# Optimization experiments

Hardware: AMD Instinct MI355X
Metric: run time of the kernel (lower is better)

## Reference

```python
import jax, jax.numpy as jnp
import numpy as np

B, LQ, LKV = 32, 512, 512
SIZE, H = 512, 8
HD = SIZE // H
SCALE = 1.0 / np.sqrt(HD)
LN_EPS = 1e-5


def layer_norm(x, w, b):
    mu = jnp.mean(x, axis=-1, keepdims=True)
    var = jnp.mean(jnp.square(x - mu), axis=-1, keepdims=True)
    return (x - mu) * jax.lax.rsqrt(var + LN_EPS) * w + b


def setup_inputs() -> dict:
    key = jax.random.key(0)
    ks = jax.random.split(key, 8)
    s = 0.02
    return {
        "query": jax.random.normal(ks[0], (B, LQ, SIZE), jnp.float32),
        "key_value": jax.random.normal(ks[1], (B, LKV, SIZE), jnp.float32),
        "Wq": jax.random.normal(ks[2], (SIZE, SIZE), jnp.float32) * s,
        "bq": jnp.zeros((SIZE,), jnp.float32),
        "Wk": jax.random.normal(ks[3], (SIZE, SIZE), jnp.float32) * s,
        "bk": jnp.zeros((SIZE,), jnp.float32),
        "Wv": jax.random.normal(ks[4], (SIZE, SIZE), jnp.float32) * s,
        "bv": jnp.zeros((SIZE,), jnp.float32),
        "Wo": jax.random.normal(ks[5], (SIZE, SIZE), jnp.float32) * s,
        "bo": jnp.zeros((SIZE,), jnp.float32),
        "ln0_w": jnp.ones((SIZE,), jnp.float32),
        "ln0_b": jnp.zeros((SIZE,), jnp.float32),
        "ln1_w": jnp.ones((SIZE,), jnp.float32),
        "ln1_b": jnp.zeros((SIZE,), jnp.float32),
    }


def reference(query, key_value, Wq, bq, Wk, bk, Wv, bv, Wo, bo, ln0_w, ln0_b, ln1_w, ln1_b):
    b, lq, _ = query.shape
    lkv = key_value.shape[1]
    # projections
    q = query @ Wq.T + bq          # [B, Lq, SIZE]
    k = key_value @ Wk.T + bk      # [B, Lkv, SIZE]
    v = key_value @ Wv.T + bv
    # split heads: torch cat(split(head_size, 2), 0) == [B,L,H,HD] view with head axis separate
    qh = q.reshape(b, lq, H, HD)
    kh = k.reshape(b, lkv, H, HD)
    vh = v.reshape(b, lkv, H, HD)
    # attention scores [B, H, Lq, Lkv]
    A_ = jnp.einsum("bqhd,bkhd->bhqk", qh, kh) * SCALE
    # signed softmax: tanh(A_) * softmax(sqrt(A_^2 + 0.01)) over keys
    A = jnp.tanh(A_) * jax.nn.softmax(jnp.sqrt(jnp.square(A_) + 0.01), axis=-1)
    # residual q + attention output, merge heads back
    oh = qh + jnp.einsum("bhqk,bkhd->bqhd", A, vh)   # [B, Lq, H, HD]
    output = oh.reshape(b, lq, SIZE)
    output = layer_norm(output, ln0_w, ln0_b)
    output = output + jax.nn.relu(output @ Wo.T + bo)
    output = layer_norm(output, ln1_w, ln1_b)
    return output
```

## Files before the change

### kernel.cpp

```cpp
#include <hip/hip_runtime.h>

#define SIZE_D 512
#define HEADS  8
#define HDIM   64
#define BATCH  32
#define SEQ    512
#define SCALE_F 0.125f
#define NROWS  (BATCH * SEQ)

typedef __attribute__((ext_vector_type(8))) short bf16x8;
typedef __attribute__((ext_vector_type(4))) float f32x4;
typedef __attribute__((ext_vector_type(4))) unsigned int u32x4;

__device__ __forceinline__ unsigned short f2bf(float f) {
    union { float f; unsigned int u; } c{f};
    unsigned int x = c.u;
    x += 0x7fffu + ((x >> 16) & 1u);
    return (unsigned short)(x >> 16);
}
__device__ __forceinline__ float bf2f(unsigned short u) {
    union { unsigned int i; float f; } c;
    c.i = (unsigned int)u << 16;
    return c.f;
}
__device__ __forceinline__ unsigned int pack2bf(float lo, float hi) {
    return ((__float_as_uint(hi) + 0x8000u) & 0xffff0000u) |
           ((__float_as_uint(lo) + 0x8000u) >> 16);
}
__device__ __forceinline__ void gload_lds16(const unsigned short* g, unsigned short* l) {
    __builtin_amdgcn_global_load_lds(
        (const __attribute__((address_space(1))) unsigned int*)g,
        (__attribute__((address_space(3))) unsigned int*)l, 16, 0, 0);
}

__global__ __launch_bounds__(256) void cvt_w4(const float* __restrict__ w0,
                                              const float* __restrict__ w1,
                                              const float* __restrict__ w2,
                                              const float* __restrict__ w3,
                                              unsigned short* __restrict__ d) {
    const float* srcs[4] = {w0, w1, w2, w3};
    const float* s = srcs[blockIdx.y];
    unsigned short* dst = d + (size_t)blockIdx.y * (SIZE_D * SIZE_D);
    const int n = SIZE_D * SIZE_D;
    const int stride = gridDim.x * blockDim.x * 4;
    for (int i = (blockIdx.x * blockDim.x + threadIdx.x) * 4; i < n; i += stride) {
        const float4 v = *reinterpret_cast<const float4*>(s + i);
        ushort4 o;
        o.x = f2bf(v.x); o.y = f2bf(v.y); o.z = f2bf(v.z); o.w = f2bf(v.w);
        *reinterpret_cast<ushort4*>(dst + i) = o;
    }
}

__global__ __launch_bounds__(256, 2) void gemm_proj3(const float* __restrict__ query,
                                                     const float* __restrict__ keyv,
                                                     const unsigned short* __restrict__ Wall,
                                                     const float* __restrict__ bq,
                                                     const float* __restrict__ bk,
                                                     const float* __restrict__ bv,
                                                     unsigned short* __restrict__ Qh,
                                                     unsigned short* __restrict__ Kh,
                                                     unsigned short* __restrict__ Vt) {
    __shared__ __align__(16) unsigned short Ad[4][128 * 32];
    __shared__ __align__(16) unsigned short Bd[4][128 * 32];

    const int tid  = threadIdx.x;
    const int wv   = tid >> 6;
    const int lane = tid & 63;
    const int g    = lane >> 4;
    const int y    = blockIdx.y;
    const int bm   = blockIdx.x * 128;
    const int bn   = y * 128;
    const int wr   = wv >> 1;
    const int wc   = wv & 1;

    const float* A = (y < 4) ? query : keyv;

    float4 areg[2][2][2];

    auto loadA = [&](int t, int slot) {
        const int k0 = t * 32;
#pragma unroll
        for (int i = 0; i < 2; ++i) {
            const int o   = i * 4096 + tid * 16;
            const int row = o >> 6;
            const int col = ((o & 63) ^ (((row >> 1) & 3) << 4)) >> 1;
            const float* src = A + (size_t)(bm + row) * SIZE_D + k0 + col;
            areg[slot][i][0] = *reinterpret_cast<const float4*>(src);
            areg[slot][i][1] = *reinterpret_cast<const float4*>(src + 4);
        }
    };
    auto writeA = [&](int buf, int slot) {
#pragma unroll
        for (int i = 0; i < 2; ++i) {
            const int o = i * 4096 + tid * 16;
            union { unsigned int u[4]; bf16x8 v; } pk;
            pk.u[0] = pack2bf(areg[slot][i][0].x, areg[slot][i][0].y);
            pk.u[1] = pack2bf(areg[slot][i][0].z, areg[slot][i][0].w);
            pk.u[2] = pack2bf(areg[slot][i][1].x, areg[slot][i][1].y);
            pk.u[3] = pack2bf(areg[slot][i][1].z, areg[slot][i][1].w);
            *reinterpret_cast<bf16x8*>(&Ad[buf][o >> 1]) = pk.v;
        }
    };
    auto stageW = [&](int buf, int t) {
        const int k0 = t * 32;
#pragma unroll
        for (int i = 0; i < 2; ++i) {
            const int o   = i * 4096 + tid * 16;
            const int row = o >> 6;
            const int col = ((o & 63) ^ (((row >> 1) & 3) << 4)) >> 1;
            gload_lds16(Wall + (size_t)(bn + row) * SIZE_D + k0 + col, &Bd[buf][o >> 1]);
        }
    };

    f32x4 acc[4][4];
#pragma unroll
    for (int mt = 0; mt < 4; ++mt)
#pragma unroll
        for (int nt = 0; nt < 4; ++nt) acc[mt][nt] = (f32x4){0.f, 0.f, 0.f, 0.f};

    auto compute = [&](int buf) {
        bf16x8 af[4], bfr[4];
#pragma unroll
        for (int mt = 0; mt < 4; ++mt) {
            const int r = wr * 64 + mt * 16 + (lane & 15);
            int byte = r * 64 + g * 16;
            byte ^= ((r >> 1) & 3) << 4;
            af[mt] = *reinterpret_cast<const bf16x8*>(
                reinterpret_cast<const char*>(&Ad[buf][0]) + byte);
        }
#pragma unroll
        for (int nt = 0; nt < 4; ++nt) {
            const int r = wc * 64 + nt * 16 + (lane & 15);
            int byte = r * 64 + g * 16;
            byte ^= ((r >> 1) & 3) << 4;
            bfr[nt] = *reinterpret_cast<const bf16x8*>(
                reinterpret_cast<const char*>(&Bd[buf][0]) + byte);
        }
#pragma unroll
        for (int mt = 0; mt < 4; ++mt)
#pragma unroll
            for (int nt = 0; nt < 4; ++nt)
                acc[mt][nt] = __builtin_amdgcn_mfma_f32_16x16x32_bf16(
                    af[mt], bfr[nt], acc[mt][nt], 0, 0, 0);
    };

    loadA(0, 0);
    loadA(1, 1);
    stageW(0, 0);
    stageW(1, 1);
    writeA(0, 0);
    writeA(1, 1);
    __syncthreads();

    for (int tt = 0; tt < 16; tt += 2) {
        if (tt < 14) {
            loadA(tt + 2, 0);
            loadA(tt + 3, 1);
            stageW((tt + 2) & 3, tt + 2);
            stageW((tt + 3) & 3, tt + 3);
        }

        compute(tt & 3);
        if (tt < 14) writeA((tt + 2) & 3, 0);
        compute((tt + 1) & 3);
        if (tt < 14) writeA((tt + 3) & 3, 1);

        __syncthreads();
    }

    if (y < 8) {
        const float* bias = (y < 4) ? bq : bk;
        unsigned short* D = (y < 4) ? Qh : Kh;
        const int coff = (y < 4) ? 0 : 512;
#pragma unroll
        for (int nt = 0; nt < 4; ++nt) {
            const int colL = bn - coff + wc * 64 + nt * 16 + (lane & 15);
            const float bc = bias[colL];
            const int h = colL >> 6, dd = colL & 63;
#pragma unroll
            for (int mt = 0; mt < 4; ++mt) {
                const int row0 = bm + wr * 64 + mt * 16 + g * 4;
#pragma unroll
                for (int r = 0; r < 4; ++r) {
                    const int row = row0 + r;
                    const int b_ = row >> 9, l = row & 511;
                    float z = acc[mt][nt][r] + bc;
                    if (y >= 4) z *= SCALE_F;
                    D[(((size_t)b_ * HEADS + h) * SEQ + l) * HDIM + dd] = f2bf(z);
                }
            }
        }
    } else {
#pragma unroll
        for (int nt = 0; nt < 4; ++nt) {
            const int c2 = bn - 1024 + wc * 64 + nt * 16 + (lane & 15);
            const float bc = bv[c2];
            const int hV = c2 >> 6, dV = c2 & 63;
#pragma unroll
            for (int mt = 0; mt < 4; ++mt) {
                const int row0 = bm + wr * 64 + mt * 16 + g * 4;
                const int b_ = row0 >> 9, kv = row0 & 511;
                ushort4 pk;
                pk.x = f2bf(acc[mt][nt][0] + bc);
                pk.y = f2bf(acc[mt][nt][1] + bc);
                pk.z = f2bf(acc[mt][nt][2] + bc);
                pk.w = f2bf(acc[mt][nt][3] + bc);
                *reinterpret_cast<ushort4*>(
                    &Vt[(((size_t)b_ * HEADS + hV) * HDIM + dV) * SEQ + kv]) = pk;
            }
        }
    }
}

__global__ __launch_bounds__(256, 2) void attn_mfma(const unsigned short* __restrict__ Qh,
                                                    const unsigned short* __restrict__ Kh,
                                                    const unsigned short* __restrict__ Vt,
                                                    unsigned short* __restrict__ outb) {
    __shared__ __align__(16) unsigned short Kt[4][64 * 64];
    __shared__ __align__(16) unsigned short Vs[4][64 * 64];

    const int tid  = threadIdx.x;
    const int wv   = tid >> 6;
    const int lane = tid & 63;
    const int bh   = blockIdx.x;
    const int b    = bh >> 3;
    const int h    = bh & 7;
    const int g    = lane >> 4;

    const unsigned short* Qb = Qh + (size_t)bh * (SEQ * HDIM);
    const unsigned short* Kb = Kh + (size_t)bh * (SEQ * HDIM);
    const unsigned short* Vb = Vt + (size_t)bh * (HDIM * SEQ);

    const int m0 = blockIdx.y * 256 + wv * 64;

    auto stageKV = [&](int buf, int t) {
        const int kv0 = t * 64;
#pragma unroll
        for (int i = 0; i < 2; ++i) {
            const int o   = i * 4096 + tid * 16;
            const int row = o >> 7;
            const int in  = (o & 127) ^ ((row & 7) << 4);
            gload_lds16(Kb + (size_t)(kv0 + row) * HDIM + (in >> 1), &Kt[buf][o >> 1]);
            gload_lds16(Vb + (size_t)row * SEQ + kv0 + (in >> 1), &Vs[buf][o >> 1]);
        }
    };

    bf16x8 qf[4][2];
#pragma unroll
    for (int mt = 0; mt < 4; ++mt)
#pragma unroll
        for (int kc = 0; kc < 2; ++kc) {
            const int m = m0 + mt * 16 + (lane & 15);
            union { u32x4 u; bf16x8 v; } cv;
            cv.u = *reinterpret_cast<const u32x4*>(
                Qb + (size_t)m * HDIM + kc * 32 + g * 8);
            qf[mt][kc] = cv.v;
        }

    f32x4 oacc[4][4];
    float esum[4] = {0.f, 0.f, 0.f, 0.f};
#pragma unroll
    for (int mt = 0; mt < 4; ++mt)
#pragma unroll
        for (int x = 0; x < 4; ++x) oacc[mt][x] = (f32x4){0.f, 0.f, 0.f, 0.f};

    stageKV(0, 0);
    stageKV(1, 1);
    __syncthreads();

    for (int tt = 0; tt < 8; tt += 2) {
        if (tt < 6) {
            stageKV((tt + 2) & 3, tt + 2);
            stageKV((tt + 3) & 3, tt + 3);
        }

#pragma unroll
        for (int p = 0; p < 2; ++p) {
            const int cur = (tt + p) & 3;

            f32x4 sacc[4][4];
#pragma unroll
            for (int nt = 0; nt < 4; ++nt)
#pragma unroll
                for (int mt = 0; mt < 4; ++mt) sacc[nt][mt] = (f32x4){0.f, 0.f, 0.f, 0.f};

#pragma unroll
            for (int kc = 0; kc < 2; ++kc) {
                bf16x8 kf[4];
#pragma unroll
                for (int nt = 0; nt < 4; ++nt) {
                    const int kvl = nt * 16 + (lane & 15);
                    int byte = kvl * 128 + kc * 64 + g * 16;
                    byte ^= (kvl & 7) << 4;
                    kf[nt] = *reinterpret_cast<const bf16x8*>(
                        reinterpret_cast<const char*>(&Kt[cur][0]) + byte);
                }
                __builtin_amdgcn_s_setprio(1);
#pragma unroll
                for (int nt = 0; nt < 4; ++nt)
#pragma unroll
                    for (int mt = 0; mt < 4; ++mt)
                        sacc[nt][mt] = __builtin_amdgcn_mfma_f32_16x16x32_bf16(
                            kf[nt], qf[mt][kc], sacc[nt][mt], 0, 0, 0);
                __builtin_amdgcn_s_setprio(0);
            }

            bf16x8 pa[2][4];
#pragma unroll
            for (int c = 0; c < 2; ++c)
#pragma unroll
                for (int mt = 0; mt < 4; ++mt) {
                    float w[8];
#pragma unroll
                    for (int j = 0; j < 8; ++j) {
                        const float s  = sacc[2 * c + (j >> 2)][mt][j & 3];
                        const float a  = fabsf(s);
                        const float tt_ = __expf(a);
                        const float t2 = tt_ * tt_;
                        const float u  = __builtin_amdgcn_sqrtf(fmaf(s, s, 0.01f));
                        const float dl = u - a;
                        const float ed = fmaf(dl, fmaf(dl, 0.5f, 1.0f), 1.0f);
                        const float eu = tt_ * ed;
                        esum[mt] += eu;
                        const float th = fmaf(-2.0f, __builtin_amdgcn_rcpf(t2 + 1.0f), 1.0f);
                        w[j] = __builtin_copysignf(th * eu, s);
                    }
                    union { unsigned int u[4]; bf16x8 v; } pk;
#pragma unroll
                    for (int pp = 0; pp < 4; ++pp)
                        pk.u[pp] = (__float_as_uint(w[2 * pp + 1]) & 0xffff0000u) |
                                   (__float_as_uint(w[2 * pp]) >> 16);
                    pa[c][mt] = pk.v;
                }

#pragma unroll
            for (int c = 0; c < 2; ++c) {
                bf16x8 vf[4];
#pragma unroll
                for (int dt = 0; dt < 4; ++dt) {
                    const int d = dt * 16 + (lane & 15);
                    const int swz = (d & 7) << 4;
                    const int rowb = d * 128;
                    uint2 lo = *reinterpret_cast<const uint2*>(
                        reinterpret_cast<const char*>(&Vs[cur][0]) +
                        (rowb + (((c * 32 + 4 * g) * 2) ^ swz)));
                    uint2 hi = *reinterpret_cast<const uint2*>(
                        reinterpret_cast<const char*>(&Vs[cur][0]) +
                        (rowb + (((c * 32 + 16 + 4 * g) * 2) ^ swz)));
                    union { unsigned int u[4]; bf16x8 v; } cvb;
                    cvb.u[0] = lo.x; cvb.u[1] = lo.y;
                    cvb.u[2] = hi.x; cvb.u[3] = hi.y;
                    vf[dt] = cvb.v;
                }
                __builtin_amdgcn_s_setprio(1);
#pragma unroll
                for (int mt = 0; mt < 4; ++mt)
#pragma unroll
                    for (int dt = 0; dt < 4; ++dt)
                        oacc[mt][dt] = __builtin_amdgcn_mfma_f32_16x16x32_bf16(
                            pa[c][mt], vf[dt], oacc[mt][dt], 0, 0, 0);
                __builtin_amdgcn_s_setprio(0);
            }
        }

        __syncthreads();
    }

    float rden[4];
#pragma unroll
    for (int mt = 0; mt < 4; ++mt) {
        float e = esum[mt];
        e += __shfl_xor(e, 16);
        e += __shfl_xor(e, 32);
        rden[mt] = __builtin_amdgcn_rcpf(e);
    }
    float rr_[4][4];
#pragma unroll
    for (int mt = 0; mt < 4; ++mt)
#pragma unroll
        for (int r = 0; r < 4; ++r)
            rr_[mt][r] = __shfl(rden[mt], g * 4 + r);

#pragma unroll
    for (int mt = 0; mt < 4; ++mt)
#pragma unroll
        for (int dt = 0; dt < 4; ++dt)
#pragma unroll
            for (int r = 0; r < 4; ++r) {
                const int m = m0 + mt * 16 + g * 4 + r;
                const int d = dt * 16 + (lane & 15);
                const float qv = bf2f(Qb[(size_t)m * HDIM + d]);
                outb[((size_t)b * SEQ + m) * SIZE_D + h * HDIM + d] =
                    f2bf(qv + oacc[mt][dt][r] * rr_[mt][r]);
            }
}

__global__ __launch_bounds__(256) void ln0_bf16(const unsigned short* __restrict__ in,
                                                const float* __restrict__ w,
                                                const float* __restrict__ b,
                                                unsigned short* __restrict__ outb) {
    const int tid  = threadIdx.x;
    const int lane = tid & 63;
    const int row  = blockIdx.x * 4 + (tid >> 6);
    const size_t base = (size_t)row * SIZE_D + lane * 8;

    const ushort4 a0 = *reinterpret_cast<const ushort4*>(&in[base]);
    const ushort4 a1 = *reinterpret_cast<const ushort4*>(&in[base + 4]);
    float x[8];
    x[0] = bf2f(a0.x); x[1] = bf2f(a0.y); x[2] = bf2f(a0.z); x[3] = bf2f(a0.w);
    x[4] = bf2f(a1.x); x[5] = bf2f(a1.y); x[6] = bf2f(a1.z); x[7] = bf2f(a1.w);

    float s = 0.f, sq = 0.f;
#pragma unroll
    for (int j = 0; j < 8; ++j) { s += x[j]; sq += x[j] * x[j]; }
#pragma unroll
    for (int off = 32; off > 0; off >>= 1) {
        s  += __shfl_xor(s, off);
        sq += __shfl_xor(sq, off);
    }

    const float mu  = s * (1.0f / SIZE_D);
    const float var = sq * (1.0f / SIZE_D) - mu * mu;
    const float rr  = rsqrtf(var + 1e-5f);

    const float4 w0 = *reinterpret_cast<const float4*>(&w[lane * 8]);
    const float4 w1 = *reinterpret_cast<const float4*>(&w[lane * 8 + 4]);
    const float4 b0 = *reinterpret_cast<const float4*>(&b[lane * 8]);
    const float4 b1 = *reinterpret_cast<const float4*>(&b[lane * 8 + 4]);
    const float wa[8] = {w0.x, w0.y, w0.z, w0.w, w1.x, w1.y, w1.z, w1.w};
    const float ba[8] = {b0.x, b0.y, b0.z, b0.w, b1.x, b1.y, b1.z, b1.w};

    union { unsigned short s[8]; bf16x8 v; } o;
#pragma unroll
    for (int j = 0; j < 8; ++j)
        o.s[j] = f2bf((x[j] - mu) * rr * wa[j] + ba[j]);
    *reinterpret_cast<bf16x8*>(&outb[base]) = o.v;
}

__global__ __launch_bounds__(512, 2) void oproj_ln(const unsigned short* __restrict__ X,
                                                   const unsigned short* __restrict__ W,
                                                   const float* __restrict__ bo,
                                                   const float* __restrict__ g1,
                                                   const float* __restrict__ b1,
                                                   float* __restrict__ out) {
    __shared__ __align__(16) unsigned short Ad[2][32 * 32];
    __shared__ __align__(16) unsigned short Bd[2][512 * 32];
    __shared__ float red[32][8][2];
    __shared__ float stat[32][2];

    const int tid  = threadIdx.x;
    const int wv   = tid >> 6;
    const int lane = tid & 63;
    const int bm   = blockIdx.x * 32;

    auto stage = [&](int buf, int t) {
        const int k0 = t * 32;
        if (tid < 128) {
            const int o   = tid * 16;
            const int row = o >> 6;
            const int in  = (o & 63) ^ (((row >> 1) & 3) << 4);
            gload_lds16(X + (size_t)(bm + row) * SIZE_D + k0 + (in >> 1), &Ad[buf][o >> 1]);
        }
#pragma unroll
        for (int i = 0; i < 4; ++i) {
            const int o   = i * 8192 + tid * 16;
            const int row = o >> 6;
            const int in  = (o & 63) ^ (((row >> 1) & 3) << 4);
            gload_lds16(W + (size_t)row * SIZE_D + k0 + (in >> 1), &Bd[buf][o >> 1]);
        }
    };

    f32x4 acc[2][4];
#pragma unroll
    for (int mt = 0; mt < 2; ++mt)
#pragma unroll
        for (int nt = 0; nt < 4; ++nt) acc[mt][nt] = (f32x4){0.f, 0.f, 0.f, 0.f};

    stage(0, 0);
    __syncthreads();
    int cur = 0;

    for (int t = 0; t < 16; ++t) {
        if (t < 15) stage(cur ^ 1, t + 1);

        bf16x8 af[2], bfr[4];
#pragma unroll
        for (int mt = 0; mt < 2; ++mt) {
            const int r = mt * 16 + (lane & 15);
            int byte = r * 64 + (lane >> 4) * 16;
            byte ^= ((r >> 1) & 3) << 4;
            af[mt] = *reinterpret_cast<const bf16x8*>(
                reinterpret_cast<const char*>(&Ad[cur][0]) + byte);
        }
#pragma unroll
        for (int nt = 0; nt < 4; ++nt) {
            const int r = wv * 64 + nt * 16 + (lane & 15);
            int byte = r * 64 + (lane >> 4) * 16;
            byte ^= ((r >> 1) & 3) << 4;
            bfr[nt] = *reinterpret_cast<const bf16x8*>(
                reinterpret_cast<const char*>(&Bd[cur][0]) + byte);
        }
#pragma unroll
        for (int mt = 0; mt < 2; ++mt)
#pragma unroll
            for (int nt = 0; nt < 4; ++nt)
                acc[mt][nt] = __builtin_amdgcn_mfma_f32_16x16x32_bf16(
                    af[mt], bfr[nt], acc[mt][nt], 0, 0, 0);

        __syncthreads();
        cur ^= 1;
    }

#pragma unroll
    for (int nt = 0; nt < 4; ++nt) {
        const int n  = wv * 64 + nt * 16 + (lane & 15);
        const float bc = bo[n];
#pragma unroll
        for (int mt = 0; mt < 2; ++mt) {
            const int row0 = bm + mt * 16 + (lane >> 4) * 4;
#pragma unroll
            for (int r = 0; r < 4; ++r) {
                const float R = bf2f(X[(size_t)(row0 + r) * SIZE_D + n]);
                acc[mt][nt][r] = R + fmaxf(acc[mt][nt][r] + bc, 0.0f);
            }
        }
    }

    float ps[2][4], pq[2][4];
#pragma unroll
    for (int mt = 0; mt < 2; ++mt)
#pragma unroll
        for (int r = 0; r < 4; ++r) {
            float s = 0.f, q = 0.f;
#pragma unroll
            for (int nt = 0; nt < 4; ++nt) {
                const float v = acc[mt][nt][r];
                s += v; q += v * v;
            }
#pragma unroll
            for (int off = 1; off <= 8; off <<= 1) {
                s += __shfl_xor(s, off);
                q += __shfl_xor(q, off);
            }
            ps[mt][r] = s; pq[mt][r] = q;
        }
    if ((lane & 15) < 8) {
        const int mtw = (lane & 15) >> 2;
        const int rw  = lane & 3;
        const int rowL = mtw * 16 + (lane >> 4) * 4 + rw;
        red[rowL][wv][0] = ps[mtw][rw];
        red[rowL][wv][1] = pq[mtw][rw];
    }
    __syncthreads();
    if (tid < 32) {
        float s = 0.f, q = 0.f;
#pragma unroll
        for (int w8 = 0; w8 < 8; ++w8) { s += red[tid][w8][0]; q += red[tid][w8][1]; }
        const float mu  = s * (1.0f / SIZE_D);
        const float var = q * (1.0f / SIZE_D) - mu * mu;
        stat[tid][0] = mu;
        stat[tid][1] = rsqrtf(var + 1e-5f);
    }
    __syncthreads();

#pragma unroll
    for (int nt = 0; nt < 4; ++nt) {
        const int n = wv * 64 + nt * 16 + (lane & 15);
        const float g = g1[n], bb = b1[n];
#pragma unroll
        for (int mt = 0; mt < 2; ++mt) {
#pragma unroll
            for (int r = 0; r < 4; ++r) {
                const int rowL = mt * 16 + (lane >> 4) * 4 + r;
                const float y = (acc[mt][nt][r] - stat[rowL][0]) * stat[rowL][1];
                out[(size_t)(bm + rowL) * SIZE_D + n] = y * g + bb;
            }
        }
    }
}

extern "C" void kernel_launch(void* const* d_in, const int* in_sizes, int n_in,
                              void* d_out, int out_size, void* d_ws, size_t ws_size,
                              hipStream_t stream) {
    const float* query = (const float*)d_in[0];
    const float* keyv  = (const float*)d_in[1];
    const float* Wq    = (const float*)d_in[2];
    const float* bq    = (const float*)d_in[3];
    const float* Wk    = (const float*)d_in[4];
    const float* bk    = (const float*)d_in[5];
    const float* Wv    = (const float*)d_in[6];
    const float* bv    = (const float*)d_in[7];
    const float* Wo    = (const float*)d_in[8];
    const float* bo    = (const float*)d_in[9];
    const float* ln0w  = (const float*)d_in[10];
    const float* ln0b  = (const float*)d_in[11];
    const float* ln1w  = (const float*)d_in[12];
    const float* ln1b  = (const float*)d_in[13];
    float* out = (float*)d_out;

    char* ws = (char*)d_ws;
    unsigned short* obf  = (unsigned short*)ws;
    unsigned short* Qh   = (unsigned short*)(ws + ((size_t)32 << 20));
    unsigned short* Xbf  = Qh;
    unsigned short* Kh   = (unsigned short*)(ws + ((size_t)48 << 20));
    unsigned short* Vt   = (unsigned short*)(ws + ((size_t)64 << 20));
    unsigned short* Wbf  = (unsigned short*)(ws + ((size_t)80 << 20));
    unsigned short* WoB  = Wbf + 786432;

    cvt_w4<<<dim3(64, 4), 256, 0, stream>>>(Wq, Wk, Wv, Wo, Wbf);

    gemm_proj3<<<dim3(128, 12), 256, 0, stream>>>(query, keyv, Wbf, bq, bk, bv, Qh, Kh, Vt);

    attn_mfma<<<dim3(BATCH * HEADS, 2), 256, 0, stream>>>(Qh, Kh, Vt, obf);

    ln0_bf16<<<NROWS / 4, 256, 0, stream>>>(obf, ln0w, ln0b, Xbf);

    oproj_ln<<<NROWS / 32, 512, 0, stream>>>(Xbf, WoB, bo, ln1w, ln1b, out);
}
```

Measured before the change: 151.9 us.

## Pre-convert activations to bf16 and stream both GEMM operands via async LDS loads

Adds a separate kernel that converts query and key_value to bf16 up front. The projection GEMM then loads both A and W tiles with global_load_lds straight into a 4-deep LDS ring, synchronised by explicit waitcnt/barrier macros. Previously the fp32 activations were loaded into registers, packed to bf16 and written to LDS inside the loop. MFMA sections also get raised wave priority. The aim is to remove register staging and conversion from the GEMM's critical path, at the cost of an extra pass that writes and rereads 32 MB of bf16 activations.

Result: no change. 152.8 us (+0.6%).

```diff
diff --git a/kernel.cpp b/kernel.cpp
--- a/kernel.cpp
+++ b/kernel.cpp
@@ -23,14 +23,39 @@
     c.i = (unsigned int)u << 16;
     return c.f;
 }
-__device__ __forceinline__ unsigned int pack2bf(float lo, float hi) {
-    return ((__float_as_uint(hi) + 0x8000u) & 0xffff0000u) |
-           ((__float_as_uint(lo) + 0x8000u) >> 16);
-}
 __device__ __forceinline__ void gload_lds16(const unsigned short* g, unsigned short* l) {
     __builtin_amdgcn_global_load_lds(
         (const __attribute__((address_space(1))) unsigned int*)g,
         (__attribute__((address_space(3))) unsigned int*)l, 16, 0, 0);
+}
+
+#define KBAR4() do {                                                      \
+    asm volatile("s_waitcnt vmcnt(4) lgkmcnt(0)" ::: "memory");           \
+    __builtin_amdgcn_sched_barrier(0);                                    \
+    __builtin_amdgcn_s_barrier();                                         \
+    __builtin_amdgcn_sched_barrier(0);                                    \
+} while (0)
+#define KBAR0() do {                                                      \
+    asm volatile("s_waitcnt vmcnt(0) lgkmcnt(0)" ::: "memory");           \
+    __builtin_amdgcn_sched_barrier(0);                                    \
+    __builtin_amdgcn_s_barrier();                                         \
+    __builtin_amdgcn_sched_barrier(0);                                    \
+} while (0)
+
+__global__ __launch_bounds__(256) void cvt_act(const float* __restrict__ q,
+                                               const float* __restrict__ kv,
+                                               unsigned short* __restrict__ dq,
+                                               unsigned short* __restrict__ dkv) {
+    const float* s = blockIdx.y ? kv : q;
+    unsigned short* d = blockIdx.y ? dkv : dq;
+    const int n = NROWS * SIZE_D;
+    const int stride = gridDim.x * blockDim.x * 4;
+    for (int i = (blockIdx.x * blockDim.x + threadIdx.x) * 4; i < n; i += stride) {
+        const float4 v = *reinterpret_cast<const float4*>(s + i);
+        ushort4 o;
+        o.x = f2bf(v.x); o.y = f2bf(v.y); o.z = f2bf(v.z); o.w = f2bf(v.w);
+        *reinterpret_cast<ushort4*>(d + i) = o;
+    }
 }
 
 __global__ __launch_bounds__(256) void cvt_w4(const float* __restrict__ w0,
@@ -51,8 +76,8 @@
     }
 }
 
-__global__ __launch_bounds__(256, 2) void gemm_proj3(const float* __restrict__ query,
-                                                     const float* __restrict__ keyv,
+__global__ __launch_bounds__(256, 2) void gemm_proj3(const unsigned short* __restrict__ Qbf,
+                                                     const unsigned short* __restrict__ KVbf,
                                                      const unsigned short* __restrict__ Wall,
                                                      const float* __restrict__ bq,
                                                      const float* __restrict__ bk,
@@ -73,41 +98,16 @@
     const int wr   = wv >> 1;
     const int wc   = wv & 1;
 
-    const float* A = (y < 4) ? query : keyv;
-
-    float4 areg[2][2][2];
-
-    auto loadA = [&](int t, int slot) {
+    const unsigned short* A = (y < 4) ? Qbf : KVbf;
+
+    auto stage = [&](int buf, int t) {
         const int k0 = t * 32;
 #pragma unroll
         for (int i = 0; i < 2; ++i) {
             const int o   = i * 4096 + tid * 16;
             const int row = o >> 6;
             const int col = ((o & 63) ^ (((row >> 1) & 3) << 4)) >> 1;
-            const float* src = A + (size_t)(bm + row) * SIZE_D + k0 + col;
-            areg[slot][i][0] = *reinterpret_cast<const float4*>(src);
-            areg[slot][i][1] = *reinterpret_cast<const float4*>(src + 4);
-        }
-    };
-    auto writeA = [&](int buf, int slot) {
-#pragma unroll
-        for (int i = 0; i < 2; ++i) {
-            const int o = i * 4096 + tid * 16;
-            union { unsigned int u[4]; bf16x8 v; } pk;
-            pk.u[0] = pack2bf(areg[slot][i][0].x, areg[slot][i][0].y);
-            pk.u[1] = pack2bf(areg[slot][i][0].z, areg[slot][i][0].w);
-            pk.u[2] = pack2bf(areg[slot][i][1].x, areg[slot][i][1].y);
-            pk.u[3] = pack2bf(areg[slot][i][1].z, areg[slot][i][1].w);
-            *reinterpret_cast<bf16x8*>(&Ad[buf][o >> 1]) = pk.v;
-        }
-    };
-    auto stageW = [&](int buf, int t) {
-        const int k0 = t * 32;
-#pragma unroll
-        for (int i = 0; i < 2; ++i) {
-            const int o   = i * 4096 + tid * 16;
-            const int row = o >> 6;
-            const int col = ((o & 63) ^ (((row >> 1) & 3) << 4)) >> 1;
+            gload_lds16(A + (size_t)(bm + row) * SIZE_D + k0 + col, &Ad[buf][o >> 1]);
             gload_lds16(Wall + (size_t)(bn + row) * SIZE_D + k0 + col, &Bd[buf][o >> 1]);
         }
     };
@@ -136,36 +136,24 @@
             bfr[nt] = *reinterpret_cast<const bf16x8*>(
                 reinterpret_cast<const char*>(&Bd[buf][0]) + byte);
         }
+        __builtin_amdgcn_s_setprio(1);
 #pragma unroll
         for (int mt = 0; mt < 4; ++mt)
 #pragma unroll
             for (int nt = 0; nt < 4; ++nt)
                 acc[mt][nt] = __builtin_amdgcn_mfma_f32_16x16x32_bf16(
                     af[mt], bfr[nt], acc[mt][nt], 0, 0, 0);
+        __builtin_amdgcn_s_setprio(0);
     };
 
-    loadA(0, 0);
-    loadA(1, 1);
-    stageW(0, 0);
-    stageW(1, 1);
-    writeA(0, 0);
-    writeA(1, 1);
-    __syncthreads();
-
-    for (int tt = 0; tt < 16; tt += 2) {
-        if (tt < 14) {
-            loadA(tt + 2, 0);
-            loadA(tt + 3, 1);
-            stageW((tt + 2) & 3, tt + 2);
-            stageW((tt + 3) & 3, tt + 3);
-        }
-
-        compute(tt & 3);
-        if (tt < 14) writeA((tt + 2) & 3, 0);
-        compute((tt + 1) & 3);
-        if (tt < 14) writeA((tt + 3) & 3, 1);
-
-        __syncthreads();
+    stage(0, 0);
+    stage(1, 1);
+
+#pragma unroll
+    for (int t = 0; t < 16; ++t) {
+        if (t < 15) { KBAR4(); } else { KBAR0(); }
+        if (t < 14) stage((t + 2) & 3, t + 2);
+        compute(t & 3);
     }
 
     if (y < 8) {
@@ -599,7 +587,9 @@
     float* out = (float*)d_out;
 
     char* ws = (char*)d_ws;
+    unsigned short* Qbf  = (unsigned short*)ws;
     unsigned short* obf  = (unsigned short*)ws;
+    unsigned short* KVbf = (unsigned short*)(ws + ((size_t)16 << 20));
     unsigned short* Qh   = (unsigned short*)(ws + ((size_t)32 << 20));
     unsigned short* Xbf  = Qh;
     unsigned short* Kh   = (unsigned short*)(ws + ((size_t)48 << 20));
@@ -607,9 +597,10 @@
     unsigned short* Wbf  = (unsigned short*)(ws + ((size_t)80 << 20));
     unsigned short* WoB  = Wbf + 786432;
 
+    cvt_act<<<dim3(1024, 2), 256, 0, stream>>>(query, keyv, Qbf, KVbf);
     cvt_w4<<<dim3(64, 4), 256, 0, stream>>>(Wq, Wk, Wv, Wo, Wbf);
 
-    gemm_proj3<<<dim3(128, 12), 256, 0, stream>>>(query, keyv, Wbf, bq, bk, bv, Qh, Kh, Vt);
+    gemm_proj3<<<dim3(128, 12), 256, 0, stream>>>(Qbf, KVbf, Wbf, bq, bk, bv, Qh, Kh, Vt);
 
     attn_mfma<<<dim3(BATCH * HEADS, 2), 256, 0, stream>>>(Qh, Kh, Vt, obf);
 
```
